# Performance work log

Hardware: AMD Instinct MI355X
Metric: run time of the kernel (lower is better)

## Reference

```python
import jax, jax.numpy as jnp
import numpy as np

B, S, ENC = 64, 2048, 1024          # batch, encoder seq len, encoder feature dim
U, E_DIM, V_SZ = 512, 256, 50000    # dec_units, embedding_dim, vocab_size
IN_DIM = ENC + E_DIM                # LSTM input: [context ; token embedding]


def setup_inputs() -> dict:
    key = jax.random.key(0)
    ks = jax.random.split(key, 16)
    g = lambda k, shp, s=0.02: (jax.random.normal(k, shp, jnp.float32) * s)
    return {
        "x": jax.random.randint(ks[0], (B, 1), 0, V_SZ),
        "c_fwd": g(ks[1], (B, U), 0.1),
        "c_bwd": g(ks[2], (B, U), 0.1),
        "enc_output": jax.random.normal(ks[3], (B, S, ENC), jnp.float32),
        "emb": g(ks[4], (V_SZ, E_DIM)),
        "W1_w": g(ks[5], (ENC, U)), "W1_b": jnp.zeros((U,), jnp.float32),
        "W2_w": g(ks[6], (U, U)),   "W2_b": jnp.zeros((U,), jnp.float32),
        "W3_w": g(ks[7], (U, U)),   "W3_b": jnp.zeros((U,), jnp.float32),
        "V_w": g(ks[8], (U, 1)),    "V_b": jnp.zeros((1,), jnp.float32),
        "Kf": g(ks[9], (IN_DIM, 4 * U)),  "bf": jnp.zeros((4 * U,), jnp.float32),
        "Kb": g(ks[10], (IN_DIM, 4 * U)), "bb": jnp.zeros((4 * U,), jnp.float32),
        "fc_w": g(ks[11], (2 * U, V_SZ)), "fc_b": jnp.zeros((V_SZ,), jnp.float32),
    }


def _lstm_step_zero_state(xin, K, b):
    # Keras LSTM single step from zero (h0, c0): recurrent term vanishes.
    # Gate order in Keras kernel: i, f, c(g), o.
    z = xin @ K + b
    i, f, g, o = jnp.split(z, 4, axis=-1)
    i, o = jax.nn.sigmoid(i), jax.nn.sigmoid(o)  # f gate multiplies c0=0
    c = i * jnp.tanh(g)
    h = o * jnp.tanh(c)
    return h, c


def reference(x, c_fwd, c_bwd, enc_output, emb,
              W1_w, W1_b, W2_w, W2_b, W3_w, W3_b, V_w, V_b,
              Kf, bf, Kb, bb, fc_w, fc_b):
    # Bahdanau additive attention: score [B, S, 1]
    hidden_proj = (c_fwd @ W2_w + W2_b + c_bwd @ W3_w + W3_b)[:, None, :]  # [B,1,U]
    score = jnp.tanh(enc_output @ W1_w + W1_b + hidden_proj) @ V_w + V_b
    attn = jax.nn.softmax(score, axis=1)                 # softmax over S
    ctx = jnp.sum(attn * enc_output, axis=1)             # [B, ENC]

    xe = emb[x[:, 0]]                                    # [B, E_DIM]
    xin = jnp.concatenate([ctx, xe], axis=-1)            # [B, ENC+E_DIM]

    # Bidirectional LSTM over a length-1 sequence from zero initial state:
    # both directions see the same single timestep with separate weights.
    hf, cf = _lstm_step_zero_state(xin, Kf, bf)
    hb, cb = _lstm_step_zero_state(xin, Kb, bb)

    out = jnp.concatenate([hf, hb], axis=-1)             # [B, 2U]
    logits = out @ fc_w + fc_b                           # [B, vocab]
    return logits, hf, cf, hb, cb
```

## Files before the change

### kernel.cpp

```cpp
#include <hip/hip_runtime.h>

using u16 = unsigned short;
typedef float f32x4 __attribute__((ext_vector_type(4)));
typedef float f32x16 __attribute__((ext_vector_type(16)));
typedef __bf16 bf16x8 __attribute__((ext_vector_type(8)));
typedef u16 u16x8 __attribute__((ext_vector_type(8)));
typedef u16 u16x4 __attribute__((ext_vector_type(4)));

static constexpr int OF_HPB   = 262144;
static constexpr int OF_CTXP  = 294912;
static constexpr int OF_STATS = 2392064;
static constexpr int OF_XIN   = 2394112;
static constexpr int OF_ZPART = 2476032;
static constexpr int OF_HHL   = 3000320;
static constexpr size_t SCRATCH_FLOATS = 3065856;
static constexpr size_t SCRATCH_BYTES  = SCRATCH_FLOATS * 4ull;

__device__ __forceinline__ u16 f2bf(float f) {
  unsigned u = __float_as_uint(f);
  u += 0x7FFFu + ((u >> 16) & 1u);
  return (u16)(u >> 16);
}
__device__ __forceinline__ float bf2f(u16 u) {
  return __uint_as_float((unsigned)u << 16);
}
__device__ __forceinline__ float fast_tanh(float x) {
  x = fminf(fmaxf(x, -20.f), 20.f);
  float e = __expf(2.f * x);
  return (e - 1.f) / (e + 1.f);
}
__device__ __forceinline__ float fast_sig(float x) { return 1.f / (1.f + __expf(-x)); }

__global__ void k_prep_w1(const float* __restrict__ W1w, u16* __restrict__ w1p) {
  __shared__ float tile[16][516];
  const int t = threadIdx.x;
  const int ks = blockIdx.x;
  {
    int kk = t >> 4, u0 = (t & 15) * 32;
    const float* src = W1w + (size_t)(ks * 16 + kk) * 512 + u0;
    #pragma unroll
    for (int i = 0; i < 8; ++i)
      *(float4*)&tile[kk][u0 + i * 4] = *(const float4*)(src + i * 4);
  }
  __syncthreads();
  #pragma unroll
  for (int q = 0; q < 4; ++q) {
    int c = t + q * 256;
    int wv = c >> 6, l = c & 63;
    int u = wv * 32 + (l & 31), koct = l >> 5;
    u16x8 p;
    #pragma unroll
    for (int e = 0; e < 8; ++e) p[e] = f2bf(tile[koct * 8 + e][u]);
    *(u16x8*)(w1p + (size_t)ks * 8192 + (size_t)c * 8) = p;
  }
}

__global__ void k_prep_hp(const float* __restrict__ cf, const float* __restrict__ cb,
                          const float* __restrict__ W2w, const float* __restrict__ W2b,
                          const float* __restrict__ W3w, const float* __restrict__ W3b,
                          const float* __restrict__ W1b, float* __restrict__ hpb) {
  __shared__ float cfl[512], cbl[512];
  const int b = blockIdx.x, t = threadIdx.x;
  cfl[t] = cf[(size_t)b * 512 + t];       cfl[t + 256] = cf[(size_t)b * 512 + t + 256];
  cbl[t] = cb[(size_t)b * 512 + t];       cbl[t + 256] = cb[(size_t)b * 512 + t + 256];
  __syncthreads();
  const int u1 = t, u2 = t + 256;
  float a1 = W2b[u1] + W3b[u1] + W1b[u1];
  float a2 = W2b[u2] + W3b[u2] + W1b[u2];
  for (int k = 0; k < 512; ++k) {
    float c1 = cfl[k], c2 = cbl[k];
    const float* r2 = W2w + (size_t)k * 512;
    const float* r3 = W3w + (size_t)k * 512;
    a1 += c1 * r2[u1] + c2 * r3[u1];
    a2 += c1 * r2[u2] + c2 * r3[u2];
  }
  hpb[(size_t)b * 512 + u1] = a1;
  hpb[(size_t)b * 512 + u2] = a2;
}

__global__ void __launch_bounds__(1024, 8)
k_attn(const float* __restrict__ enc, const u16* __restrict__ w1p,
       const float* __restrict__ hpb, const float* __restrict__ Vw,
       const float* __restrict__ Vb, float* __restrict__ ctxp,
       float* __restrict__ stats) {
  __shared__ __align__(16) u16 smem[8448];

  const int t = threadIdx.x;
  const int bid = blockIdx.x;
  const int b = bid >> 5, tile = bid & 31;
  const size_t row0 = (size_t)b * 2048 + (size_t)tile * 64;

  const int l = t & 63, wv = t >> 6;

  const u16* bbase = w1p + (size_t)wv * 512 + (size_t)l * 8;

  const int sr = t >> 2, sh = (t >> 1) & 1, sq = t & 1;
  const float* a_src = enc + (row0 + sr) * 1024 + sh * 8 + sq * 4;
  const int a_dst = ((sr >> 5) * 64 + (sr & 31) + (sh << 5)) * 8 + sq * 4;

  f32x16 acc0, acc1;
  #pragma unroll
  for (int i = 0; i < 16; ++i) { acc0[i] = 0.f; acc1[i] = 0.f; }

  float4 av = {0.f, 0.f, 0.f, 0.f};
  if (t < 256) {
    float4 p0 = *(const float4*)(a_src);
    u16x4 w4;
    w4[0] = f2bf(p0.x); w4[1] = f2bf(p0.y); w4[2] = f2bf(p0.z); w4[3] = f2bf(p0.w);
    *(u16x4*)(smem + a_dst) = w4;
    av = *(const float4*)(a_src + 16);
  }
  __syncthreads();

  #pragma unroll 2
  for (int ks = 0; ks < 64; ++ks) {
    const int cur = ks & 1;
    float4 nx = av;
    if (t < 256 && ks < 62) nx = *(const float4*)(a_src + (ks + 2) * 16);
    if (t < 256 && ks < 63) {
      u16x4 w4;
      w4[0] = f2bf(av.x); w4[1] = f2bf(av.y); w4[2] = f2bf(av.z); w4[3] = f2bf(av.w);
      *(u16x4*)(smem + ((cur ^ 1) << 10) + a_dst) = w4;
    }
    bf16x8 bfr = *(const bf16x8*)(bbase + (size_t)ks * 8192);
    const u16* Ac = smem + (cur << 10);
    bf16x8 a0 = *(const bf16x8*)(Ac + l * 8);
    bf16x8 a1 = *(const bf16x8*)(Ac + 512 + l * 8);
    acc0 = __builtin_amdgcn_mfma_f32_32x32x16_bf16(a0, bfr, acc0, 0, 0, 0);
    acc1 = __builtin_amdgcn_mfma_f32_32x32x16_bf16(a1, bfr, acc1, 0, 0, 0);
    av = nx;
    __syncthreads();
  }

  float* fsm = (float*)smem;
  float* red = fsm;
  float* scv = fsm + 1088;
  float* pcv = fsm + 1152;

  const int ucol = (wv << 5) + (l & 31);
  const float vwv = Vw[ucol];
  const float hpv = hpb[(size_t)b * 512 + ucol];
  const int hi4 = (l >> 5) * 4;
  const bool writer = ((l & 31) == 0);
  #pragma unroll
  for (int im = 0; im < 2; ++im) {
    #pragma unroll
    for (int r = 0; r < 16; ++r) {
      float s = vwv * fast_tanh((im ? acc1[r] : acc0[r]) + hpv);
      s += __shfl_xor(s, 1);
      s += __shfl_xor(s, 2);
      s += __shfl_xor(s, 4);
      s += __shfl_xor(s, 8);
      s += __shfl_xor(s, 16);
      if (writer) {
        int sl = im * 32 + (r & 3) + 8 * (r >> 2) + hi4;
        red[sl * 17 + wv] = s;
      }
    }
  }
  __syncthreads();
  if (t < 64) {
    float s = Vb[0];
    #pragma unroll
    for (int wq = 0; wq < 16; ++wq) s += red[t * 17 + wq];
    float e = __expf(s);
    scv[t] = e;
    float p = e;
    p += __shfl_xor(p, 1);  p += __shfl_xor(p, 2);  p += __shfl_xor(p, 4);
    p += __shfl_xor(p, 8);  p += __shfl_xor(p, 16); p += __shfl_xor(p, 32);
    if (t == 0) stats[bid] = p;
  }
  __syncthreads();

  {
    const int c4 = (t & 255) * 4;
    const int rq = t >> 8;
    const float* ep = enc + (row0 + rq * 16) * 1024 + c4;
    float ax = 0.f, ay = 0.f, az = 0.f, aw2 = 0.f;
    #pragma unroll 4
    for (int r = 0; r < 16; ++r) {
      float4 v = *(const float4*)(ep + (size_t)r * 1024);
      float sc = scv[rq * 16 + r];
      ax += sc * v.x; ay += sc * v.y; az += sc * v.z; aw2 += sc * v.w;
    }
    if (rq) {
      float4 st = {ax, ay, az, aw2};
      *(float4*)&pcv[(rq - 1) * 1024 + c4] = st;
    }
    __syncthreads();
    if (rq == 0) {
      float4 p1 = *(const float4*)&pcv[c4];
      float4 p2 = *(const float4*)&pcv[1024 + c4];
      float4 p3 = *(const float4*)&pcv[2048 + c4];
      float4 o = {ax + p1.x + p2.x + p3.x, ay + p1.y + p2.y + p3.y,
                  az + p1.z + p2.z + p3.z, aw2 + p1.w + p2.w + p3.w};
      *(float4*)&ctxp[(size_t)bid * 1024 + c4] = o;
    }
  }
}

__global__ void k_attn_reduce(const float* __restrict__ ctxp, const float* __restrict__ stats,
                              const int* __restrict__ x, const float* __restrict__ emb,
                              float* __restrict__ xin) {
  __shared__ float ps[32];
  __shared__ float invs;
  const int b = blockIdx.x, t = threadIdx.x;
  if (t < 32) ps[t] = stats[b * 32 + t];
  __syncthreads();
  if (t == 0) {
    float s = 0.f;
    #pragma unroll
    for (int i = 0; i < 32; ++i) s += ps[i];
    invs = 1.f / s;
  }
  __syncthreads();
  const float inv = invs;
  #pragma unroll
  for (int i = 0; i < 4; ++i) {
    int c = t + i * 256;
    float a = 0.f;
    for (int chv = 0; chv < 32; ++chv)
      a += ctxp[((size_t)b * 32 + chv) * 1024 + c];
    xin[(size_t)b * 1280 + c] = a * inv;
  }
  xin[(size_t)b * 1280 + 1024 + t] = emb[(size_t)x[b] * 256 + t];
}

__global__ void k_lstm_gemm(const float* __restrict__ xin, const float* __restrict__ Kf,
                            const float* __restrict__ Kb, float* __restrict__ zpart) {
  __shared__ float xl[32][68];
  const int t = threadIdx.x;
  const int bid = blockIdx.x;
  const int dir = bid >> 7;
  const int jt  = (bid >> 1) & 63;
  const int ks  = bid & 1;
  const float* K = dir ? Kb : Kf;
  const int j  = jt * 32 + (t & 31);
  const int tb = t >> 5;
  const int brow = t >> 2, kq = (t & 3) * 8;
  float acc[8] = {0,0,0,0,0,0,0,0};
  for (int k0 = ks * 640; k0 < ks * 640 + 640; k0 += 32) {
    float4 x0 = *(const float4*)&xin[(size_t)brow * 1280 + k0 + kq];
    float4 x1 = *(const float4*)&xin[(size_t)brow * 1280 + k0 + kq + 4];
    __syncthreads();
    xl[kq+0][brow]=x0.x; xl[kq+1][brow]=x0.y; xl[kq+2][brow]=x0.z; xl[kq+3][brow]=x0.w;
    xl[kq+4][brow]=x1.x; xl[kq+5][brow]=x1.y; xl[kq+6][brow]=x1.z; xl[kq+7][brow]=x1.w;
    __syncthreads();
    const float* Kp = K + (size_t)k0 * 2048 + j;
    #pragma unroll 8
    for (int kk = 0; kk < 32; ++kk) {
      float wv = Kp[(size_t)kk * 2048];
      float4 v0 = *(const float4*)&xl[kk][tb * 8];
      float4 v1 = *(const float4*)&xl[kk][tb * 8 + 4];
      acc[0] += v0.x * wv; acc[1] += v0.y * wv; acc[2] += v0.z * wv; acc[3] += v0.w * wv;
      acc[4] += v1.x * wv; acc[5] += v1.y * wv; acc[6] += v1.z * wv; acc[7] += v1.w * wv;
    }
  }
  float* zp = zpart + ((size_t)dir * 2 + ks) * 64 * 2048;
  #pragma unroll
  for (int i = 0; i < 8; ++i)
    zp[(size_t)(tb * 8 + i) * 2048 + j] = acc[i];
}

__global__ void k_gates(const float* __restrict__ zpart, const float* __restrict__ bfv,
                        const float* __restrict__ bbv, float* __restrict__ dout,
                        u16* __restrict__ hhl) {
  const int dir = blockIdx.x >> 6, b = blockIdx.x & 63, u = threadIdx.x;
  const float* bias = dir ? bbv : bfv;
  const float* z0 = zpart + ((size_t)dir * 2 + 0) * 131072 + (size_t)b * 2048;
  const float* z1 = zpart + ((size_t)dir * 2 + 1) * 131072 + (size_t)b * 2048;
  float zi = z0[u]        + z1[u]        + bias[u];
  float zg = z0[1024 + u] + z1[1024 + u] + bias[1024 + u];
  float zo = z0[1536 + u] + z1[1536 + u] + bias[1536 + u];
  float c = fast_sig(zi) * fast_tanh(zg);
  float h = fast_sig(zo) * fast_tanh(c);
  size_t base = 3200000u + (size_t)dir * 65536u;
  dout[base + (size_t)b * 512 + u] = h;
  dout[base + 32768u + (size_t)b * 512 + u] = c;
  u16 hi = f2bf(h);
  u16 lo = f2bf(h - bf2f(hi));
  hhl[(size_t)b * 1024 + dir * 512 + u] = hi;
  hhl[65536u + (size_t)b * 1024 + dir * 512 + u] = lo;
}

__global__ void __launch_bounds__(256)
k_fc_mfma(const float* __restrict__ fcw, const u16* __restrict__ hhl,
          const float* __restrict__ fcb, float* __restrict__ logits) {
  __shared__ float Bs[2][32 * 136];
  const int t = threadIdx.x;
  const int j0 = blockIdx.x * 128;
  const int l = t & 63, w = t >> 6;
  const int ln = l & 15, lg = l >> 4;
  const int srow = t >> 3, scol = (t & 7) * 16;
  const bool interior = (j0 + 128 <= 50000);

  f32x4 acc[4][2];
  #pragma unroll
  for (int im = 0; im < 4; ++im)
    #pragma unroll
    for (int nf = 0; nf < 2; ++nf) acc[im][nf] = f32x4{0.f, 0.f, 0.f, 0.f};

  float4 pre[4];
  {
    const float* src = fcw + (size_t)srow * 50000 + j0 + scol;
    if (interior) {
      #pragma unroll
      for (int q = 0; q < 4; ++q) pre[q] = *(const float4*)(src + q * 4);
    } else {
      #pragma unroll
      for (int q = 0; q < 4; ++q) {
        int jb = j0 + scol + q * 4;
        pre[q].x = (jb + 0 < 50000) ? src[q*4 + 0] : 0.f;
        pre[q].y = (jb + 1 < 50000) ? src[q*4 + 1] : 0.f;
        pre[q].z = (jb + 2 < 50000) ? src[q*4 + 2] : 0.f;
        pre[q].w = (jb + 3 < 50000) ? src[q*4 + 3] : 0.f;
      }
    }
    #pragma unroll
    for (int q = 0; q < 4; ++q)
      *(float4*)&Bs[0][srow * 136 + scol + q * 4] = pre[q];
  }
  __syncthreads();

  for (int ks = 0; ks < 32; ++ks) {
    const int cur = ks & 1;
    if (ks < 31) {
      const float* src = fcw + (size_t)(ks + 1) * 32 * 50000 + (size_t)srow * 50000 + j0 + scol;
      if (interior) {
        #pragma unroll
        for (int q = 0; q < 4; ++q) pre[q] = *(const float4*)(src + q * 4);
      } else {
        #pragma unroll
        for (int q = 0; q < 4; ++q) {
          int jb = j0 + scol + q * 4;
          pre[q].x = (jb + 0 < 50000) ? src[q*4 + 0] : 0.f;
          pre[q].y = (jb + 1 < 50000) ? src[q*4 + 1] : 0.f;
          pre[q].z = (jb + 2 < 50000) ? src[q*4 + 2] : 0.f;
          pre[q].w = (jb + 3 < 50000) ? src[q*4 + 3] : 0.f;
        }
      }
    }
    bf16x8 ahi[4], alo[4];
    #pragma unroll
    for (int im = 0; im < 4; ++im) {
      const u16* ha = hhl + (size_t)(im * 16 + ln) * 1024 + ks * 32 + lg * 8;
      ahi[im] = *(const bf16x8*)(ha);
      alo[im] = *(const bf16x8*)(ha + 65536);
    }
    bf16x8 bfr[2];
    #pragma unroll
    for (int nf = 0; nf < 2; ++nf) {
      u16x8 pv;
      #pragma unroll
      for (int i = 0; i < 8; ++i)
        pv[i] = f2bf(Bs[cur][(lg * 8 + i) * 136 + w * 32 + nf * 16 + ln]);
      bfr[nf] = *(bf16x8*)&pv;
    }
    #pragma unroll
    for (int im = 0; im < 4; ++im)
      #pragma unroll
      for (int nf = 0; nf < 2; ++nf) {
        acc[im][nf] = __builtin_amdgcn_mfma_f32_16x16x32_bf16(alo[im], bfr[nf], acc[im][nf], 0, 0, 0);
        acc[im][nf] = __builtin_amdgcn_mfma_f32_16x16x32_bf16(ahi[im], bfr[nf], acc[im][nf], 0, 0, 0);
      }
    if (ks < 31) {
      #pragma unroll
      for (int q = 0; q < 4; ++q)
        *(float4*)&Bs[cur ^ 1][srow * 136 + scol + q * 4] = pre[q];
    }
    __syncthreads();
  }

  #pragma unroll
  for (int nf = 0; nf < 2; ++nf) {
    int c = j0 + w * 32 + nf * 16 + ln;
    if (c < 50000) {
      float fb = fcb[c];
      #pragma unroll
      for (int im = 0; im < 4; ++im)
        #pragma unroll
        for (int r = 0; r < 4; ++r) {
          int row = im * 16 + lg * 4 + r;
          logits[(size_t)row * 50000 + c] = acc[im][nf][r] + fb;
        }
    }
  }
}

__global__ void __launch_bounds__(256)
k_fc_f32(const float* __restrict__ dout_ro, const float* __restrict__ fcw,
         const float* __restrict__ fcb, float* __restrict__ logits) {
  __shared__ float ol[64][68];
  __shared__ float wl[64][132];
  const int t = threadIdx.x;
  const int j0 = blockIdx.x * 128;
  const int tb = t >> 5, tj = t & 31;
  const float* hf = dout_ro + 3200000u;
  const float* hb = dout_ro + 3200000u + 65536u;
  float acc[8][4];
  #pragma unroll
  for (int bi = 0; bi < 8; ++bi)
    #pragma unroll
    for (int ji = 0; ji < 4; ++ji) acc[bi][ji] = 0.f;

  for (int k0 = 0; k0 < 1024; k0 += 64) {
    __syncthreads();
    {
      int bb = t >> 2, kq = (t & 3) * 16;
      const float* src = (k0 < 512) ? (hf + (size_t)bb * 512 + k0 + kq)
                                    : (hb + (size_t)bb * 512 + (k0 - 512) + kq);
      #pragma unroll
      for (int i = 0; i < 4; ++i) {
        float4 v = *(const float4*)(src + i * 4);
        ol[kq + i*4 + 0][bb] = v.x;
        ol[kq + i*4 + 1][bb] = v.y;
        ol[kq + i*4 + 2][bb] = v.z;
        ol[kq + i*4 + 3][bb] = v.w;
      }
    }
    {
      int kk = t >> 2, jh = (t & 3) * 32;
      const float* wsrc = fcw + (size_t)(k0 + kk) * 50000 + j0 + jh;
      #pragma unroll
      for (int i = 0; i < 8; ++i) {
        int j = j0 + jh + i * 4;
        float4 v;
        if (j + 3 < 50000) {
          v = *(const float4*)(wsrc + i * 4);
        } else {
          v.x = (j + 0 < 50000) ? wsrc[i*4 + 0] : 0.f;
          v.y = (j + 1 < 50000) ? wsrc[i*4 + 1] : 0.f;
          v.z = (j + 2 < 50000) ? wsrc[i*4 + 2] : 0.f;
          v.w = 0.f;
        }
        *(float4*)&wl[kk][jh + i * 4] = v;
      }
    }
    __syncthreads();
    #pragma unroll 4
    for (int kk = 0; kk < 64; ++kk) {
      float4 wv = *(const float4*)&wl[kk][tj * 4];
      float4 q0 = *(const float4*)&ol[kk][tb * 8];
      float4 q1 = *(const float4*)&ol[kk][tb * 8 + 4];
      float obv[8] = {q0.x, q0.y, q0.z, q0.w, q1.x, q1.y, q1.z, q1.w};
      #pragma unroll
      for (int bi = 0; bi < 8; ++bi) {
        acc[bi][0] += obv[bi] * wv.x;
        acc[bi][1] += obv[bi] * wv.y;
        acc[bi][2] += obv[bi] * wv.z;
        acc[bi][3] += obv[bi] * wv.w;
      }
    }
  }

  const int j = j0 + tj * 4;
  if (j + 3 < 50000) {
    float4 fb = *(const float4*)(fcb + j);
    #pragma unroll
    for (int bi = 0; bi < 8; ++bi) {
      float4 r;
      r.x = acc[bi][0] + fb.x; r.y = acc[bi][1] + fb.y;
      r.z = acc[bi][2] + fb.z; r.w = acc[bi][3] + fb.w;
      *(float4*)&logits[(size_t)(tb * 8 + bi) * 50000 + j] = r;
    }
  } else {
    for (int ji = 0; ji < 4; ++ji) {
      if (j + ji < 50000) {
        float fb = fcb[j + ji];
        for (int bi = 0; bi < 8; ++bi)
          logits[(size_t)(tb * 8 + bi) * 50000 + j + ji] = acc[bi][ji] + fb;
      }
    }
  }
}

extern "C" void kernel_launch(void* const* d_in, const int* in_sizes, int n_in,
                              void* d_out, int out_size, void* d_ws, size_t ws_size,
                              hipStream_t stream) {
  const int*   x    = (const int*)  d_in[0];
  const float* cfwd = (const float*)d_in[1];
  const float* cbwd = (const float*)d_in[2];
  const float* enc  = (const float*)d_in[3];
  const float* emb  = (const float*)d_in[4];
  const float* W1w  = (const float*)d_in[5];
  const float* W1b  = (const float*)d_in[6];
  const float* W2w  = (const float*)d_in[7];
  const float* W2b  = (const float*)d_in[8];
  const float* W3w  = (const float*)d_in[9];
  const float* W3b  = (const float*)d_in[10];
  const float* Vw   = (const float*)d_in[11];
  const float* Vb   = (const float*)d_in[12];
  const float* Kf   = (const float*)d_in[13];
  const float* bfv  = (const float*)d_in[14];
  const float* Kb   = (const float*)d_in[15];
  const float* bbv  = (const float*)d_in[16];
  const float* fcw  = (const float*)d_in[17];
  const float* fcb  = (const float*)d_in[18];
  float* out = (float*)d_out;

  const bool haveWs = (ws_size >= SCRATCH_BYTES);
  float* S = haveWs ? (float*)d_ws : out;
  u16*   w1p   = (u16*)S;
  float* hpb   = S + OF_HPB;
  float* ctxp  = S + OF_CTXP;
  float* stats = S + OF_STATS;
  float* xin   = S + OF_XIN;
  float* zpart = S + OF_ZPART;
  u16*   hhl   = (u16*)(S + OF_HHL);

  k_prep_w1<<<64, 256, 0, stream>>>(W1w, w1p);
  k_prep_hp<<<64, 256, 0, stream>>>(cfwd, cbwd, W2w, W2b, W3w, W3b, W1b, hpb);
  k_attn<<<2048, 1024, 0, stream>>>(enc, w1p, hpb, Vw, Vb, ctxp, stats);
  k_attn_reduce<<<64, 256, 0, stream>>>(ctxp, stats, x, emb, xin);
  k_lstm_gemm<<<256, 256, 0, stream>>>(xin, Kf, Kb, zpart);
  k_gates<<<128, 512, 0, stream>>>(zpart, bfv, bbv, out, hhl);
  if (haveWs) k_fc_mfma<<<392, 256, 0, stream>>>(fcw, hhl, fcb, out);
  else        k_fc_f32<<<391, 256, 0, stream>>>(out, fcw, fcb, out);
}
```

Measured before the change: 549.7 us.

## Stage full enc tile in LDS once and reuse it for the context sum

The attention kernel now loads a 32-row encoder tile in full, converting it to bf16 into LDS (64KB) up front. It reuses that copy for the context weighted sum instead of rereading enc from global memory, which removes the second read of enc. Partial contexts are stored as bf16, and the grid doubles to 4096 blocks with 64 partials per batch. The costs are large LDS use, which lowers occupancy, no overlap between the global loads and the MFMA loop, and lower precision in the context partials.

Result: no change. 544.4 us (-1.0%).

```diff
diff --git a/kernel.cpp b/kernel.cpp
--- a/kernel.cpp
+++ b/kernel.cpp
@@ -10,10 +10,10 @@
 static constexpr int OF_HPB   = 262144;
 static constexpr int OF_CTXP  = 294912;
 static constexpr int OF_STATS = 2392064;
-static constexpr int OF_XIN   = 2394112;
-static constexpr int OF_ZPART = 2476032;
-static constexpr int OF_HHL   = 3000320;
-static constexpr size_t SCRATCH_FLOATS = 3065856;
+static constexpr int OF_XIN   = 2396160;
+static constexpr int OF_ZPART = 2478080;
+static constexpr int OF_HHL   = 3002368;
+static constexpr size_t SCRATCH_FLOATS = 3067904;
 static constexpr size_t SCRATCH_BYTES  = SCRATCH_FLOATS * 4ull;
 
 __device__ __forceinline__ u16 f2bf(float f) {
@@ -81,61 +81,50 @@
 __global__ void __launch_bounds__(1024, 8)
 k_attn(const float* __restrict__ enc, const u16* __restrict__ w1p,
        const float* __restrict__ hpb, const float* __restrict__ Vw,
-       const float* __restrict__ Vb, float* __restrict__ ctxp,
+       const float* __restrict__ Vb, u16* __restrict__ ctxp,
        float* __restrict__ stats) {
-  __shared__ __align__(16) u16 smem[8448];
+  __shared__ __align__(16) u16 As[32768];
+  __shared__ float epi[3648];
 
   const int t = threadIdx.x;
   const int bid = blockIdx.x;
-  const int b = bid >> 5, tile = bid & 31;
-  const size_t row0 = (size_t)b * 2048 + (size_t)tile * 64;
+  const int b = bid >> 6, tile = bid & 63;
+  const size_t row0 = (size_t)b * 2048 + (size_t)tile * 32;
 
   const int l = t & 63, wv = t >> 6;
 
+  {
+    const int r = t >> 5, cl = t & 31;
+    const float* src = enc + (row0 + r) * 1024 + cl * 4;
+    #pragma unroll
+    for (int i = 0; i < 8; ++i) {
+      float4 v = *(const float4*)(src + i * 128);
+      const int c0 = i * 128 + cl * 4;
+      u16x4 w4;
+      w4[0] = f2bf(v.x); w4[1] = f2bf(v.y); w4[2] = f2bf(v.z); w4[3] = f2bf(v.w);
+      *(u16x4*)(As + (c0 >> 4) * 512 + (((c0 >> 3) & 1) * 32 + r) * 8 + (c0 & 7)) = w4;
+    }
+  }
+  __syncthreads();
+
   const u16* bbase = w1p + (size_t)wv * 512 + (size_t)l * 8;
-
-  const int sr = t >> 2, sh = (t >> 1) & 1, sq = t & 1;
-  const float* a_src = enc + (row0 + sr) * 1024 + sh * 8 + sq * 4;
-  const int a_dst = ((sr >> 5) * 64 + (sr & 31) + (sh << 5)) * 8 + sq * 4;
-
-  f32x16 acc0, acc1;
-  #pragma unroll
-  for (int i = 0; i < 16; ++i) { acc0[i] = 0.f; acc1[i] = 0.f; }
-
-  float4 av = {0.f, 0.f, 0.f, 0.f};
-  if (t < 256) {
-    float4 p0 = *(const float4*)(a_src);
-    u16x4 w4;
-    w4[0] = f2bf(p0.x); w4[1] = f2bf(p0.y); w4[2] = f2bf(p0.z); w4[3] = f2bf(p0.w);
-    *(u16x4*)(smem + a_dst) = w4;
-    av = *(const float4*)(a_src + 16);
-  }
-  __syncthreads();
-
-  #pragma unroll 2
+  f32x16 acc;
+  #pragma unroll
+  for (int i = 0; i < 16; ++i) acc[i] = 0.f;
+
+  bf16x8 b0 = *(const bf16x8*)(bbase);
+  bf16x8 b1 = *(const bf16x8*)(bbase + 8192);
+  #pragma unroll 4
   for (int ks = 0; ks < 64; ++ks) {
-    const int cur = ks & 1;
-    float4 nx = av;
-    if (t < 256 && ks < 62) nx = *(const float4*)(a_src + (ks + 2) * 16);
-    if (t < 256 && ks < 63) {
-      u16x4 w4;
-      w4[0] = f2bf(av.x); w4[1] = f2bf(av.y); w4[2] = f2bf(av.z); w4[3] = f2bf(av.w);
-      *(u16x4*)(smem + ((cur ^ 1) << 10) + a_dst) = w4;
-    }
-    bf16x8 bfr = *(const bf16x8*)(bbase + (size_t)ks * 8192);
-    const u16* Ac = smem + (cur << 10);
-    bf16x8 a0 = *(const bf16x8*)(Ac + l * 8);
-    bf16x8 a1 = *(const bf16x8*)(Ac + 512 + l * 8);
-    acc0 = __builtin_amdgcn_mfma_f32_32x32x16_bf16(a0, bfr, acc0, 0, 0, 0);
-    acc1 = __builtin_amdgcn_mfma_f32_32x32x16_bf16(a1, bfr, acc1, 0, 0, 0);
-    av = nx;
-    __syncthreads();
-  }
-
-  float* fsm = (float*)smem;
-  float* red = fsm;
-  float* scv = fsm + 1088;
-  float* pcv = fsm + 1152;
+    bf16x8 a = *(const bf16x8*)(As + ks * 512 + l * 8);
+    acc = __builtin_amdgcn_mfma_f32_32x32x16_bf16(a, b0, acc, 0, 0, 0);
+    b0 = b1;
+    if (ks < 62) b1 = *(const bf16x8*)(bbase + (size_t)(ks + 2) * 8192);
+  }
+
+  float* red = epi;
+  float* scv = epi + 544;
+  float* pcv = epi + 576;
 
   const int ucol = (wv << 5) + (l & 31);
   const float vwv = Vw[ucol];
@@ -143,23 +132,20 @@
   const int hi4 = (l >> 5) * 4;
   const bool writer = ((l & 31) == 0);
   #pragma unroll
-  for (int im = 0; im < 2; ++im) {
-    #pragma unroll
-    for (int r = 0; r < 16; ++r) {
-      float s = vwv * fast_tanh((im ? acc1[r] : acc0[r]) + hpv);
-      s += __shfl_xor(s, 1);
-      s += __shfl_xor(s, 2);
-      s += __shfl_xor(s, 4);
-      s += __shfl_xor(s, 8);
-      s += __shfl_xor(s, 16);
-      if (writer) {
-        int sl = im * 32 + (r & 3) + 8 * (r >> 2) + hi4;
-        red[sl * 17 + wv] = s;
-      }
-    }
-  }
-  __syncthreads();
-  if (t < 64) {
+  for (int r = 0; r < 16; ++r) {
+    float s = vwv * fast_tanh(acc[r] + hpv);
+    s += __shfl_xor(s, 1);
+    s += __shfl_xor(s, 2);
+    s += __shfl_xor(s, 4);
+    s += __shfl_xor(s, 8);
+    s += __shfl_xor(s, 16);
+    if (writer) {
+      int sl = (r & 3) + 8 * (r >> 2) + hi4;
+      red[sl * 17 + wv] = s;
+    }
+  }
+  __syncthreads();
+  if (t < 32) {
     float s = Vb[0];
     #pragma unroll
     for (int wq = 0; wq < 16; ++wq) s += red[t * 17 + wq];
@@ -167,7 +153,7 @@
     scv[t] = e;
     float p = e;
     p += __shfl_xor(p, 1);  p += __shfl_xor(p, 2);  p += __shfl_xor(p, 4);
-    p += __shfl_xor(p, 8);  p += __shfl_xor(p, 16); p += __shfl_xor(p, 32);
+    p += __shfl_xor(p, 8);  p += __shfl_xor(p, 16);
     if (t == 0) stats[bid] = p;
   }
   __syncthreads();
@@ -175,13 +161,15 @@
   {
     const int c4 = (t & 255) * 4;
     const int rq = t >> 8;
-    const float* ep = enc + (row0 + rq * 16) * 1024 + c4;
+    const int ks = c4 >> 4, koct = (c4 >> 3) & 1, e0 = c4 & 7;
     float ax = 0.f, ay = 0.f, az = 0.f, aw2 = 0.f;
-    #pragma unroll 4
-    for (int r = 0; r < 16; ++r) {
-      float4 v = *(const float4*)(ep + (size_t)r * 1024);
-      float sc = scv[rq * 16 + r];
-      ax += sc * v.x; ay += sc * v.y; az += sc * v.z; aw2 += sc * v.w;
+    #pragma unroll
+    for (int r = 0; r < 8; ++r) {
+      const int row = rq * 8 + r;
+      u16x4 v = *(const u16x4*)(As + ks * 512 + (koct * 32 + row) * 8 + e0);
+      float sc = scv[row];
+      ax += sc * bf2f(v[0]); ay += sc * bf2f(v[1]);
+      az += sc * bf2f(v[2]); aw2 += sc * bf2f(v[3]);
     }
     if (rq) {
       float4 st = {ax, ay, az, aw2};
@@ -192,36 +180,41 @@
       float4 p1 = *(const float4*)&pcv[c4];
       float4 p2 = *(const float4*)&pcv[1024 + c4];
       float4 p3 = *(const float4*)&pcv[2048 + c4];
-      float4 o = {ax + p1.x + p2.x + p3.x, ay + p1.y + p2.y + p3.y,
-                  az + p1.z + p2.z + p3.z, aw2 + p1.w + p2.w + p3.w};
-      *(float4*)&ctxp[(size_t)bid * 1024 + c4] = o;
-    }
-  }
-}
-
-__global__ void k_attn_reduce(const float* __restrict__ ctxp, const float* __restrict__ stats,
+      u16x4 o;
+      o[0] = f2bf(ax + p1.x + p2.x + p3.x);
+      o[1] = f2bf(ay + p1.y + p2.y + p3.y);
+      o[2] = f2bf(az + p1.z + p2.z + p3.z);
+      o[3] = f2bf(aw2 + p1.w + p2.w + p3.w);
+      *(u16x4*)(ctxp + (size_t)bid * 1024 + c4) = o;
+    }
+  }
+}
+
+__global__ void k_attn_reduce(const u16* __restrict__ ctxp, const float* __restrict__ stats,
                               const int* __restrict__ x, const float* __restrict__ emb,
                               float* __restrict__ xin) {
-  __shared__ float ps[32];
+  __shared__ float ps[64];
   __shared__ float invs;
   const int b = blockIdx.x, t = threadIdx.x;
-  if (t < 32) ps[t] = stats[b * 32 + t];
+  if (t < 64) ps[t] = stats[b * 64 + t];
   __syncthreads();
   if (t == 0) {
     float s = 0.f;
     #pragma unroll
-    for (int i = 0; i < 32; ++i) s += ps[i];
+    for (int i = 0; i < 64; ++i) s += ps[i];
     invs = 1.f / s;
   }
   __syncthreads();
   const float inv = invs;
-  #pragma unroll
-  for (int i = 0; i < 4; ++i) {
-    int c = t + i * 256;
-    float a = 0.f;
-    for (int chv = 0; chv < 32; ++chv)
-      a += ctxp[((size_t)b * 32 + chv) * 1024 + c];
-    xin[(size_t)b * 1280 + c] = a * inv;
+  {
+    const int c4 = t * 4;
+    float a0 = 0.f, a1 = 0.f, a2 = 0.f, a3 = 0.f;
+    for (int ch = 0; ch < 64; ++ch) {
+      u16x4 v = *(const u16x4*)(ctxp + ((size_t)b * 64 + ch) * 1024 + c4);
+      a0 += bf2f(v[0]); a1 += bf2f(v[1]); a2 += bf2f(v[2]); a3 += bf2f(v[3]);
+    }
+    float4 o = {a0 * inv, a1 * inv, a2 * inv, a3 * inv};
+    *(float4*)&xin[(size_t)b * 1280 + c4] = o;
   }
   xin[(size_t)b * 1280 + 1024 + t] = emb[(size_t)x[b] * 256 + t];
 }
@@ -502,7 +495,7 @@
   float* S = haveWs ? (float*)d_ws : out;
   u16*   w1p   = (u16*)S;
   float* hpb   = S + OF_HPB;
-  float* ctxp  = S + OF_CTXP;
+  u16*   ctxp  = (u16*)(S + OF_CTXP);
   float* stats = S + OF_STATS;
   float* xin   = S + OF_XIN;
   float* zpart = S + OF_ZPART;
@@ -510,7 +503,7 @@
 
   k_prep_w1<<<64, 256, 0, stream>>>(W1w, w1p);
   k_prep_hp<<<64, 256, 0, stream>>>(cfwd, cbwd, W2w, W2b, W3w, W3b, W1b, hpb);
-  k_attn<<<2048, 1024, 0, stream>>>(enc, w1p, hpb, Vw, Vb, ctxp, stats);
+  k_attn<<<4096, 1024, 0, stream>>>(enc, w1p, hpb, Vw, Vb, ctxp, stats);
   k_attn_reduce<<<64, 256, 0, stream>>>(ctxp, stats, x, emb, xin);
   k_lstm_gemm<<<256, 256, 0, stream>>>(xin, Kf, Kb, zpart);
   k_gates<<<128, 512, 0, stream>>>(zpart, bfv, bbv, out, hhl);
```
